# Optimization experiments

Hardware: AMD Instinct MI355X
Metric: run time of the kernel (lower is better)

The kernel has to match this reference:

```python
import jax, jax.numpy as jnp
import numpy as np

N, E = 8192, 131072
NS, NV = 128, 64            # scalar (0e) / vector (1o) multiplicities
D = NS + 3 * NV             # 320 node feature dim
EA = 20                     # edge_attr_dim
HID = 128
WNUM = NS + NS + NV + NV    # 384 per-edge tensor-product weights
EPS = 1e-5


def _split(x):
    return x[:, :NS], x[:, NS:].reshape(x.shape[0], NV, 3)


def _merge(s, v):
    return jnp.concatenate([s, v.reshape(v.shape[0], -1)], axis=-1)


def _o3_linear(x, ws, bs, wv):
    # per-irrep linear: scalars get bias, vectors are channel-mixed only
    s, v = _split(x)
    return _merge(s @ ws + bs, jnp.einsum('ncm,cd->ndm', v, wv))


def _normgate(x):
    # silu on scalars; vectors gated by silu(norm)/norm (equivariant)
    s, v = _split(x)
    n = jnp.sqrt(jnp.sum(v * v, axis=-1) + EPS * EPS)
    return _merge(jax.nn.silu(s), v * (jax.nn.silu(n) / n)[:, :, None])


def setup_inputs() -> dict:
    key = jax.random.key(0)
    ks = jax.random.split(key, 24)
    rn = lambda k, sh, sc=1.0: jax.random.normal(k, sh, dtype=jnp.float32) * sc
    inp = {
        'node_feat': rn(ks[0], (N, D)),
        'edge_attr': rn(ks[1], (E, EA)),
        'edge_rshs': rn(ks[2], (E, 4)),
        'edge_index': jax.random.randint(ks[3], (2, E), 0, N, dtype=jnp.int32),
        # lin_node0 / lin_node1 (o3.Linear on 128x0e+64x1o)
        'lin0_ws': rn(ks[4], (NS, NS), 1 / np.sqrt(NS)),
        'lin0_bs': jnp.zeros((NS,), jnp.float32),
        'lin0_wv': rn(ks[5], (NV, NV), 1 / np.sqrt(NV)),
        'lin1_ws': rn(ks[6], (NS, NS), 1 / np.sqrt(NS)),
        'lin1_bs': jnp.zeros((NS,), jnp.float32),
        'lin1_wv': rn(ks[7], (NV, NV), 1 / np.sqrt(NV)),
        # lin_node2: tp_out (192x0e + 192x1o) -> node_out (128x0e + 64x1o)
        'lin2_ws': rn(ks[8], (NS + NV, NS), 1 / np.sqrt(NS + NV)),
        'lin2_bs': jnp.zeros((NS,), jnp.float32),
        'lin2_wv': rn(ks[9], (NS + NV, NV), 1 / np.sqrt(NS + NV)),
        # lin_edge_scalar MLP: (2*NS + NV = 320) -> 128 -> WNUM
        'es_w1': rn(ks[10], (2 * NS + NV, HID), 1 / np.sqrt(2 * NS + NV)),
        'es_b1': jnp.zeros((HID,), jnp.float32),
        'es_w2': rn(ks[11], (HID, WNUM), 1 / np.sqrt(HID)),
        'es_b2': jnp.zeros((WNUM,), jnp.float32),
        # lin_edge_rbf MLP: EA -> 128 -> WNUM
        'er_w1': rn(ks[12], (EA, HID), 1 / np.sqrt(EA)),
        'er_b1': jnp.zeros((HID,), jnp.float32),
        'er_w2': rn(ks[13], (HID, WNUM), 1 / np.sqrt(HID)),
        'er_b2': jnp.zeros((WNUM,), jnp.float32),
        # EquivariantLayerNorm affine params
        'ln_gs': jnp.ones((NS,), jnp.float32),
        'ln_bs': jnp.zeros((NS,), jnp.float32),
        'ln_gv': jnp.ones((NS + NV,), jnp.float32),
    }
    return inp


def reference(node_feat, edge_attr, edge_rshs, edge_index,
              lin0_ws, lin0_bs, lin0_wv, lin1_ws, lin1_bs, lin1_wv,
              lin2_ws, lin2_bs, lin2_wv,
              es_w1, es_b1, es_w2, es_b2, er_w1, er_b1, er_w2, er_b2,
              ln_gs, ln_bs, ln_gv):
    n_nodes = node_feat.shape[0]
    recv, send = edge_index[0], edge_index[1]

    # lin_node0 + EquivariantDot (keep only the 1o channel dots) -> edge scalars s0
    pre = _o3_linear(node_feat, lin0_ws, lin0_bs, lin0_wv)
    ps, pv = _split(pre)
    vdot = jnp.einsum('ecm,ecm->ec', pv[recv], pv[send])          # [E, NV]
    s0 = jnp.concatenate([ps[recv], ps[send], vdot], axis=-1)     # [E, 320]

    # normgate -> lin_node1 -> gather sender features
    x = _o3_linear(_normgate(node_feat), lin1_ws, lin1_bs, lin1_wv)
    xs, xv = _split(x)
    xs_j, xv_j = xs[send], xv[send]

    # per-edge tensor-product weights: MLP(s0) * MLP(edge_attr)
    w = (jax.nn.silu(s0 @ es_w1 + es_b1) @ es_w2 + es_b2) * \
        (jax.nn.silu(edge_attr @ er_w1 + er_b1) @ er_w2 + er_b2)  # [E, 384]
    w1, w2 = w[:, :NS], w[:, NS:2 * NS]
    w3, w4 = w[:, 2 * NS:2 * NS + NV], w[:, 2 * NS + NV:]

    y0 = edge_rshs[:, :1]    # l=0 SH  [E,1]
    y1 = edge_rshs[:, 1:4]   # l=1 SH  [E,3]

    # uvu weighted tensor product paths (path_normalization='none')
    m_s1 = xs_j * y0 * w1                                                   # 0e x 0e -> 0e [E,NS]
    m_s2 = jnp.einsum('ecm,em->ec', xv_j, y1) * w4 * (1.0 / np.sqrt(3.0))   # 1o x 1o -> 0e [E,NV]
    m_v1 = xs_j[:, :, None] * y1[:, None, :] * w2[:, :, None]               # 0e x 1o -> 1o [E,NS,3]
    m_v2 = xv_j * (y0 * w3)[:, :, None]                                     # 1o x 0e -> 1o [E,NV,3]

    msg_s = jnp.concatenate([m_s1, m_s2], axis=-1)       # [E, NS+NV]
    msg_v = jnp.concatenate([m_v1, m_v2], axis=1)        # [E, NS+NV, 3]

    # scatter-add messages to receiving nodes
    acc_s = jax.ops.segment_sum(msg_s, recv, num_segments=n_nodes)
    acc_v = jax.ops.segment_sum(msg_v, recv, num_segments=n_nodes)

    # lin_node2: mix tp_out channels down to node_out
    os = acc_s @ lin2_ws + lin2_bs                        # [N, NS]
    ov = jnp.einsum('ncm,cd->ndm', acc_v, lin2_wv)        # [N, NV, 3]

    # EquivariantLayerNorm: standard LN on scalars, RMS-of-norms on vectors
    mu = jnp.mean(os, axis=-1, keepdims=True)
    var = jnp.var(os, axis=-1, keepdims=True)
    os = (os - mu) / jnp.sqrt(var + EPS) * ln_gs + ln_bs
    n2 = jnp.mean(jnp.sum(ov * ov, axis=-1), axis=-1, keepdims=True)  # [N,1]
    ov = ov / jnp.sqrt(n2 + EPS)[:, :, None] * ln_gv[NS:][None, :, None]

    # residual update (irreps_in == irreps_out)
    return node_feat + _merge(os, ov)
```

## Files before the change

### kernel.cpp

```cpp
#include <hip/hip_runtime.h>
#include <hip/hip_bf16.h>

typedef __bf16 bf16_t;
typedef __bf16 v8bf __attribute__((ext_vector_type(8)));
typedef __bf16 v2bf __attribute__((ext_vector_type(2)));
typedef __bf16 v4bf __attribute__((ext_vector_type(4)));
typedef float  v16f __attribute__((ext_vector_type(16)));

#define NSC   128
#define NVC   64
#define DDIM  320
#define HIDN  128
#define WNUM  384
#define S0STR 328
#define HSTR  136

__device__ __forceinline__ float siluf(float x) { return x / (1.f + __expf(-x)); }

__global__ void k_wconv(const float* __restrict__ esw1, const float* __restrict__ esw2,
                        const float* __restrict__ erw1, const float* __restrict__ erw2,
                        bf16_t* __restrict__ p1, bf16_t* __restrict__ p2,
                        bf16_t* __restrict__ p3, bf16_t* __restrict__ p4)
{
    const int gid = blockIdx.x * blockDim.x + threadIdx.x;
    const int stride = gridDim.x * blockDim.x;
    for (int i = gid; i < 80*512; i += stride) {
        int frag = i >> 9, q = i & 511, lane = q >> 3, j = q & 7;
        int kc = frag >> 2, nt = frag & 3;
        int n = nt*32 + (lane & 31), k = kc*16 + (lane >> 5)*8 + j;
        p1[i] = (bf16_t)esw1[k*128 + n];
    }
    for (int i = gid; i < 8*512; i += stride) {
        int frag = i >> 9, q = i & 511, lane = q >> 3, j = q & 7;
        int kc = frag >> 2, nt = frag & 3;
        int n = nt*32 + (lane & 31), k = kc*16 + (lane >> 5)*8 + j;
        p3[i] = (k < 20) ? (bf16_t)erw1[k*128 + n] : (bf16_t)(0.f);
    }
    for (int i = gid; i < 96*512; i += stride) {
        int frag = i >> 9, q = i & 511, lane = q >> 3, j = q & 7;
        int ch = frag >> 5, kc = (frag >> 2) & 7, nt = frag & 3;
        int n = ch*128 + nt*32 + (lane & 31), k = kc*16 + (lane >> 5)*8 + j;
        p2[i] = (bf16_t)esw2[k*384 + n];
        p4[i] = (bf16_t)erw2[k*384 + n];
    }
}

__global__ void k_hist(const int* __restrict__ eidx, int* __restrict__ hist, int E)
{
    for (int e = blockIdx.x * blockDim.x + threadIdx.x; e < E; e += gridDim.x * blockDim.x)
        atomicAdd(&hist[eidx[e]], 1);
}

__global__ __launch_bounds__(1024) void k_scan(const int* __restrict__ hist,
                                               int* __restrict__ off, int* __restrict__ cnt, int N)
{
    __shared__ int part[1024];
    const int tid = threadIdx.x;
    const int C = (N + 1023) >> 10;
    const int base = tid * C;
    int s = 0;
    for (int j = 0; j < C; ++j) { int idx = base + j; if (idx < N) s += hist[idx]; }
    part[tid] = s;
    __syncthreads();
    for (int d = 1; d < 1024; d <<= 1) {
        int u = (tid >= d) ? part[tid - d] : 0;
        __syncthreads();
        part[tid] += u;
        __syncthreads();
    }
    int run = part[tid] - s;
    for (int j = 0; j < C; ++j) {
        int idx = base + j;
        if (idx < N) { off[idx] = run; cnt[idx] = run; run += hist[idx]; }
    }
    if (tid == 1023) off[N] = part[1023];
}

__global__ void k_scatter(const int* __restrict__ eidx, const float* __restrict__ rshs,
                          const float* __restrict__ ea_g, int* __restrict__ cnt,
                          int* __restrict__ nsort, int* __restrict__ send_p,
                          float4* __restrict__ rshs_p, bf16_t* __restrict__ ea32, int E)
{
    for (int e = blockIdx.x * blockDim.x + threadIdx.x; e < E; e += gridDim.x * blockDim.x) {
        int n = eidx[e];
        int pos = atomicAdd(&cnt[n], 1);
        nsort[pos] = n;
        send_p[pos] = eidx[E + e];
        rshs_p[pos] = *(const float4*)(rshs + (size_t)e*4);
        const float* src = ea_g + (size_t)e*20;
        bf16_t tmp[32];
        #pragma unroll
        for (int j = 0; j < 20; ++j) tmp[j] = (bf16_t)src[j];
        #pragma unroll
        for (int j = 20; j < 32; ++j) tmp[j] = (bf16_t)(0.f);
        bf16_t* dst = ea32 + (size_t)pos*32;
        #pragma unroll
        for (int q = 0; q < 4; ++q)
            *((v8bf*)dst + q) = *((const v8bf*)tmp + q);
    }
}

__global__ __launch_bounds__(256) void k_nodeprep(
    const float* __restrict__ nf,
    const float* __restrict__ w0s, const float* __restrict__ b0s, const float* __restrict__ w0v,
    const float* __restrict__ w1s, const float* __restrict__ b1s, const float* __restrict__ w1v,
    bf16_t* __restrict__ ps_bf, bf16_t* __restrict__ pv_bf,
    bf16_t* __restrict__ xs_bf, bf16_t* __restrict__ xv4, int N)
{
    __shared__ float s_in[16][128];
    __shared__ float vt[3][64][16];
    const int tid = threadIdx.x;
    const int nb = blockIdx.x * 16;
    const size_t N64 = (size_t)N * 64;

    for (int idx = tid; idx < 16*320; idx += 256) {
        int n = idx / 320, c = idx % 320;
        int gn = nb + n; if (gn >= N) gn = N - 1;
        float v = nf[(size_t)gn*320 + c];
        if (c < 128) s_in[n][c] = v;
        else { int q = c - 128; vt[q % 3][q / 3][n] = v; }
    }
    __syncthreads();

    {
        const int col = tid & 127, g = tid >> 7;
        float acc[8];
        #pragma unroll
        for (int j = 0; j < 8; ++j) acc[j] = 0.f;
        for (int c4 = 0; c4 < 128; c4 += 4) {
            float wa = w0s[(c4+0)*128 + col];
            float wb = w0s[(c4+1)*128 + col];
            float wc = w0s[(c4+2)*128 + col];
            float wd = w0s[(c4+3)*128 + col];
            #pragma unroll
            for (int j = 0; j < 8; ++j) {
                float4 sv = *(const float4*)&s_in[g*8+j][c4];
                acc[j] += sv.x*wa + sv.y*wb + sv.z*wc + sv.w*wd;
            }
        }
        float b = b0s[col];
        #pragma unroll
        for (int j = 0; j < 8; ++j) {
            int gn = nb + g*8 + j;
            if (gn < N) ps_bf[(size_t)gn*128 + col] = (bf16_t)(acc[j] + b);
        }
    }
    if (tid < 192) {
        const int d = tid & 63, m = tid >> 6;
        float acc[16];
        #pragma unroll
        for (int j = 0; j < 16; ++j) acc[j] = 0.f;
        for (int c = 0; c < 64; ++c) {
            float w = w0v[c*64 + d];
            float4 a0 = *(const float4*)&vt[m][c][0];
            float4 a1 = *(const float4*)&vt[m][c][4];
            float4 a2 = *(const float4*)&vt[m][c][8];
            float4 a3 = *(const float4*)&vt[m][c][12];
            acc[0]+=a0.x*w; acc[1]+=a0.y*w; acc[2]+=a0.z*w; acc[3]+=a0.w*w;
            acc[4]+=a1.x*w; acc[5]+=a1.y*w; acc[6]+=a1.z*w; acc[7]+=a1.w*w;
            acc[8]+=a2.x*w; acc[9]+=a2.y*w; acc[10]+=a2.z*w; acc[11]+=a2.w*w;
            acc[12]+=a3.x*w; acc[13]+=a3.y*w; acc[14]+=a3.z*w; acc[15]+=a3.w*w;
        }
        #pragma unroll
        for (int j = 0; j < 16; ++j) {
            int gn = nb + j;
            if (gn < N) pv_bf[(size_t)m*N64 + (size_t)gn*64 + d] = (bf16_t)acc[j];
        }
    }
    __syncthreads();

    for (int idx = tid; idx < 2048; idx += 256) {
        int n = idx >> 7, c = idx & 127;
        s_in[n][c] = siluf(s_in[n][c]);
    }
    for (int idx = tid; idx < 1024; idx += 256) {
        int n = idx & 15, cc = idx >> 4;
        float v0 = vt[0][cc][n], v1 = vt[1][cc][n], v2 = vt[2][cc][n];
        float nn = sqrtf(v0*v0 + v1*v1 + v2*v2 + 1e-10f);
        float sc = 1.f / (1.f + __expf(-nn));
        vt[0][cc][n] = v0*sc; vt[1][cc][n] = v1*sc; vt[2][cc][n] = v2*sc;
    }
    __syncthreads();

    {
        const int col = tid & 127, g = tid >> 7;
        float acc[8];
        #pragma unroll
        for (int j = 0; j < 8; ++j) acc[j] = 0.f;
        for (int c4 = 0; c4 < 128; c4 += 4) {
            float wa = w1s[(c4+0)*128 + col];
            float wb = w1s[(c4+1)*128 + col];
            float wc = w1s[(c4+2)*128 + col];
            float wd = w1s[(c4+3)*128 + col];
            #pragma unroll
            for (int j = 0; j < 8; ++j) {
                float4 sv = *(const float4*)&s_in[g*8+j][c4];
                acc[j] += sv.x*wa + sv.y*wb + sv.z*wc + sv.w*wd;
            }
        }
        float b = b1s[col];
        #pragma unroll
        for (int j = 0; j < 8; ++j) {
            int gn = nb + g*8 + j;
            if (gn < N) xs_bf[(size_t)gn*128 + col] = (bf16_t)(acc[j] + b);
        }
    }
    if (tid < 192) {
        const int d = tid & 63, m = tid >> 6;
        float acc[16];
        #pragma unroll
        for (int j = 0; j < 16; ++j) acc[j] = 0.f;
        for (int c = 0; c < 64; ++c) {
            float w = w1v[c*64 + d];
            float4 a0 = *(const float4*)&vt[m][c][0];
            float4 a1 = *(const float4*)&vt[m][c][4];
            float4 a2 = *(const float4*)&vt[m][c][8];
            float4 a3 = *(const float4*)&vt[m][c][12];
            acc[0]+=a0.x*w; acc[1]+=a0.y*w; acc[2]+=a0.z*w; acc[3]+=a0.w*w;
            acc[4]+=a1.x*w; acc[5]+=a1.y*w; acc[6]+=a1.z*w; acc[7]+=a1.w*w;
            acc[8]+=a2.x*w; acc[9]+=a2.y*w; acc[10]+=a2.z*w; acc[11]+=a2.w*w;
            acc[12]+=a3.x*w; acc[13]+=a3.y*w; acc[14]+=a3.z*w; acc[15]+=a3.w*w;
        }
        #pragma unroll
        for (int j = 0; j < 16; ++j) {
            int gn = nb + j;
            if (gn < N) xv4[(size_t)gn*256 + d*4 + m] = (bf16_t)acc[j];
        }
    }
}

__global__ __launch_bounds__(256) void k_edge2(
    const int* __restrict__ nsort, const int* __restrict__ send_p,
    const bf16_t* __restrict__ ea32,
    const bf16_t* __restrict__ ps_bf, const bf16_t* __restrict__ pv_bf,
    const bf16_t* __restrict__ p1, const bf16_t* __restrict__ p2,
    const bf16_t* __restrict__ p3, const bf16_t* __restrict__ p4,
    const float* __restrict__ es_b1, const float* __restrict__ es_b2,
    const float* __restrict__ er_b1, const float* __restrict__ er_b2,
    bf16_t* __restrict__ w_bf, int N, int E)
{
    __shared__ __align__(16) bf16_t s0h[32*S0STR];
    __shared__ int   recv_l[32], send_l[32];

    const int tid  = threadIdx.x;
    const int lane = tid & 63;
    const int wid  = tid >> 6;
    const int e0   = blockIdx.x * 32;
    const size_t N64 = (size_t)N * 64;

    if (tid < 32) {
        int i = e0 + tid; if (i >= E) i = E - 1;
        recv_l[tid] = nsort[i];
        send_l[tid] = send_p[i];
    }
    __syncthreads();

    #pragma unroll
    for (int rr = 0; rr < 8; ++rr) {
        int r = wid*8 + rr;
        int nr = recv_l[r], nsd = send_l[r];
        if (lane < 32) {
            *(uint2*)&s0h[r*S0STR + lane*4] = *(const uint2*)(ps_bf + (size_t)nr*NSC + lane*4);
        } else {
            int l2 = lane - 32;
            *(uint2*)&s0h[r*S0STR + 128 + l2*4] = *(const uint2*)(ps_bf + (size_t)nsd*NSC + l2*4);
        }
        float d = 0.f;
        #pragma unroll
        for (int m = 0; m < 3; ++m)
            d += (float)pv_bf[m*N64 + (size_t)nr*64 + lane] * (float)pv_bf[m*N64 + (size_t)nsd*64 + lane];
        s0h[r*S0STR + 256 + lane] = (bf16_t)d;
    }
    __syncthreads();

    const int lc = lane & 31;
    const int kh = lane >> 5;
    bf16_t* h1 = s0h;
    bf16_t* h2 = s0h + 32*HSTR;
    const int col1 = wid*32 + lc;

    v16f acc;

    #pragma unroll
    for (int j = 0; j < 16; ++j) acc[j] = 0.f;
    {
        const bf16_t* aB = &s0h[lc*S0STR + kh*8];
        #pragma unroll
        for (int kc = 0; kc < 20; ++kc) {
            v8bf a = *(const v8bf*)(aB + kc*16);
            v8bf b = *(const v8bf*)(p1 + (size_t)((kc<<2) + wid)*512 + lane*8);
            acc = __builtin_amdgcn_mfma_f32_32x32x16_bf16(a, b, acc, 0, 0, 0);
        }
    }
    __syncthreads();

    {
        const float be = es_b1[col1];
        #pragma unroll
        for (int reg = 0; reg < 16; ++reg) {
            int row = (reg & 3) + 8*(reg >> 2) + 4*kh;
            h1[row*HSTR + col1] = (bf16_t)siluf(acc[reg] + be);
        }
    }

    #pragma unroll
    for (int j = 0; j < 16; ++j) acc[j] = 0.f;
    #pragma unroll
    for (int kc = 0; kc < 2; ++kc) {
        v8bf a = *(const v8bf*)(ea32 + (size_t)(e0 + lc)*32 + kc*16 + kh*8);
        v8bf b = *(const v8bf*)(p3 + (size_t)((kc<<2) + wid)*512 + lane*8);
        acc = __builtin_amdgcn_mfma_f32_32x32x16_bf16(a, b, acc, 0, 0, 0);
    }
    {
        const float br = er_b1[col1];
        #pragma unroll
        for (int reg = 0; reg < 16; ++reg) {
            int row = (reg & 3) + 8*(reg >> 2) + 4*kh;
            h2[row*HSTR + col1] = (bf16_t)siluf(acc[reg] + br);
        }
    }
    __syncthreads();

    #pragma unroll
    for (int ch = 0; ch < 3; ++ch) {
        #pragma unroll
        for (int j = 0; j < 16; ++j) acc[j] = 0.f;
        #pragma unroll
        for (int kc = 0; kc < 8; ++kc) {
            v8bf a1 = *(const v8bf*)&h1[lc*HSTR + kc*16 + kh*8];
            v8bf b1 = *(const v8bf*)(p2 + (size_t)(((ch*8 + kc)<<2) + wid)*512 + lane*8);
            acc = __builtin_amdgcn_mfma_f32_32x32x16_bf16(a1, b1, acc, 0, 0, 0);
        }
        const int col = ch*128 + wid*32 + lc;
        const float be = es_b2[col];
        bf16_t hes[16];
        #pragma unroll
        for (int reg = 0; reg < 16; ++reg) hes[reg] = (bf16_t)(acc[reg] + be);

        #pragma unroll
        for (int j = 0; j < 16; ++j) acc[j] = 0.f;
        #pragma unroll
        for (int kc = 0; kc < 8; ++kc) {
            v8bf a2 = *(const v8bf*)&h2[lc*HSTR + kc*16 + kh*8];
            v8bf b2 = *(const v8bf*)(p4 + (size_t)(((ch*8 + kc)<<2) + wid)*512 + lane*8);
            acc = __builtin_amdgcn_mfma_f32_32x32x16_bf16(a2, b2, acc, 0, 0, 0);
        }
        const float br = er_b2[col];
        int idx;
        if (ch == 0)      idx = col*2;
        else if (ch == 1) idx = (col - 128)*2 + 1;
        else { int q = col - 256; idx = (q < 64) ? 256 + q*2 : 256 + (q - 64)*2 + 1; }
        #pragma unroll
        for (int reg = 0; reg < 16; ++reg) {
            int row = (reg & 3) + 8*(reg >> 2) + 4*kh;
            int i = e0 + row;
            if (i < E) w_bf[(size_t)i*WNUM + idx] = (bf16_t)((float)hes[reg] * (acc[reg] + br));
        }
    }
}

__global__ __launch_bounds__(192) void k_gather(
    const int* __restrict__ off, const int* __restrict__ send_p,
    const float4* __restrict__ rshs_p,
    const bf16_t* __restrict__ xs_bf, const bf16_t* __restrict__ xv4,
    const bf16_t* __restrict__ w_bf,
    const float* __restrict__ nf,
    const float* __restrict__ w2s, const float* __restrict__ b2s, const float* __restrict__ w2v,
    const float* __restrict__ ln_gs, const float* __restrict__ ln_bs, const float* __restrict__ ln_gv,
    float* __restrict__ out, int N, int E)
{
    __shared__ float accS_l[192];
    __shared__ float accV_l[576];
    __shared__ float os_l[128];
    __shared__ float ov_l[192];
    __shared__ float stats[3];
    const int tid = threadIdx.x;
    const int n = blockIdx.x;
    const int i0 = off[n], i1 = off[n+1];

    float a0 = 0.f, a1 = 0.f, a2 = 0.f, a3 = 0.f;
    float b0 = 0.f, b1 = 0.f, b2 = 0.f, b3 = 0.f;
    if (tid < 128) {
        const int c = tid;
        int i = i0;
        for (; i + 2 <= i1; i += 2) {
            int nsdA = send_p[i],   nsdB = send_p[i+1];
            float4 yA = rshs_p[i],  yB = rshs_p[i+1];
            v2bf wA = *(const v2bf*)(w_bf + (size_t)i*WNUM + c*2);
            v2bf wB = *(const v2bf*)(w_bf + (size_t)(i+1)*WNUM + c*2);
            float xsA = (float)xs_bf[(size_t)nsdA*NSC + c];
            float xsB = (float)xs_bf[(size_t)nsdB*NSC + c];
            a0 += xsA * yA.x * (float)wA[0];
            b0 += xsB * yB.x * (float)wB[0];
            float xwA = xsA * (float)wA[1], xwB = xsB * (float)wB[1];
            a1 += xwA * yA.y; a2 += xwA * yA.z; a3 += xwA * yA.w;
            b1 += xwB * yB.y; b2 += xwB * yB.z; b3 += xwB * yB.w;
        }
        if (i < i1) {
            int nsd = send_p[i];
            float4 y = rshs_p[i];
            v2bf w = *(const v2bf*)(w_bf + (size_t)i*WNUM + c*2);
            float xs = (float)xs_bf[(size_t)nsd*NSC + c];
            a0 += xs * y.x * (float)w[0];
            float xw = xs * (float)w[1];
            a1 += xw * y.y; a2 += xw * y.z; a3 += xw * y.w;
        }
        a0 += b0; a1 += b1; a2 += b2; a3 += b3;
        accS_l[c] = a0;
        accV_l[c*3+0] = a1; accV_l[c*3+1] = a2; accV_l[c*3+2] = a3;
    } else {
        const int u = tid - 128;
        int i = i0;
        for (; i + 2 <= i1; i += 2) {
            int nsdA = send_p[i],   nsdB = send_p[i+1];
            float4 yA = rshs_p[i],  yB = rshs_p[i+1];
            v2bf wA = *(const v2bf*)(w_bf + (size_t)i*WNUM + 256 + u*2);
            v2bf wB = *(const v2bf*)(w_bf + (size_t)(i+1)*WNUM + 256 + u*2);
            v4bf xvA = *(const v4bf*)(xv4 + (size_t)nsdA*256 + u*4);
            v4bf xvB = *(const v4bf*)(xv4 + (size_t)nsdB*256 + u*4);
            float vA0 = (float)xvA[0], vA1 = (float)xvA[1], vA2 = (float)xvA[2];
            float vB0 = (float)xvB[0], vB1 = (float)xvB[1], vB2 = (float)xvB[2];
            a0 += (vA0*yA.y + vA1*yA.z + vA2*yA.w) * (float)wA[1] * 0.57735026918962576f;
            b0 += (vB0*yB.y + vB1*yB.z + vB2*yB.w) * (float)wB[1] * 0.57735026918962576f;
            float sA = yA.x * (float)wA[0], sB = yB.x * (float)wB[0];
            a1 += vA0*sA; a2 += vA1*sA; a3 += vA2*sA;
            b1 += vB0*sB; b2 += vB1*sB; b3 += vB2*sB;
        }
        if (i < i1) {
            int nsd = send_p[i];
            float4 y = rshs_p[i];
            v2bf w = *(const v2bf*)(w_bf + (size_t)i*WNUM + 256 + u*2);
            v4bf xv = *(const v4bf*)(xv4 + (size_t)nsd*256 + u*4);
            float v0 = (float)xv[0], v1 = (float)xv[1], v2 = (float)xv[2];
            a0 += (v0*y.y + v1*y.z + v2*y.w) * (float)w[1] * 0.57735026918962576f;
            float s = y.x * (float)w[0];
            a1 += v0*s; a2 += v1*s; a3 += v2*s;
        }
        a0 += b0; a1 += b1; a2 += b2; a3 += b3;
        accS_l[128+u] = a0;
        accV_l[(128+u)*3+0] = a1; accV_l[(128+u)*3+1] = a2; accV_l[(128+u)*3+2] = a3;
    }
    __syncthreads();

    for (int o = tid; o < 320; o += 192) {
        if (o < 128) {
            float acc = 0.f;
            #pragma unroll 4
            for (int c = 0; c < 192; ++c) acc += accS_l[c] * w2s[c*128 + o];
            os_l[o] = acc + b2s[o];
        } else {
            int q = o - 128;
            int m = q % 3, d = q / 3;
            float acc = 0.f;
            #pragma unroll 4
            for (int c = 0; c < 192; ++c) acc += accV_l[c*3 + m] * w2v[c*64 + d];
            ov_l[q] = acc;
        }
    }
    __syncthreads();

    if (tid < 64) {
        float x0 = os_l[tid], x1 = os_l[tid + 64];
        float s = x0 + x1;
        #pragma unroll
        for (int o = 32; o > 0; o >>= 1) s += __shfl_xor(s, o);
        float mu = s * (1.f/128.f);
        float d0 = x0 - mu, d1 = x1 - mu;
        float q = d0*d0 + d1*d1;
        #pragma unroll
        for (int o = 32; o > 0; o >>= 1) q += __shfl_xor(q, o);
        float var = q * (1.f/128.f);
        float v0 = ov_l[tid], v1 = ov_l[tid + 64], v2 = ov_l[tid + 128];
        float q2 = v0*v0 + v1*v1 + v2*v2;
        #pragma unroll
        for (int o = 32; o > 0; o >>= 1) q2 += __shfl_xor(q2, o);
        float n2 = q2 * (1.f/64.f);
        if (tid == 0) {
            stats[0] = mu;
            stats[1] = rsqrtf(var + 1e-5f);
            stats[2] = rsqrtf(n2 + 1e-5f);
        }
    }
    __syncthreads();

    const float mu = stats[0], rstd = stats[1], rn2 = stats[2];
    const size_t base = (size_t)n * DDIM;
    for (int i = tid; i < DDIM; i += 192) {
        if (i < 128) {
            out[base + i] = nf[base + i] + (os_l[i] - mu) * rstd * ln_gs[i] + ln_bs[i];
        } else {
            int o = i - 128;
            int d = o / 3;
            out[base + i] = nf[base + i] + ov_l[o] * rn2 * ln_gv[128 + d];
        }
    }
}

static inline size_t align64(size_t x) { return (x + 63) & ~(size_t)63; }

extern "C" void kernel_launch(void* const* d_in, const int* in_sizes, int n_in,
                              void* d_out, int out_size, void* d_ws, size_t ws_size,
                              hipStream_t stream)
{
    const float* nf    = (const float*)d_in[0];
    const float* ea_g  = (const float*)d_in[1];
    const float* rshs  = (const float*)d_in[2];
    const int*   eidx  = (const int*)  d_in[3];
    const float* w0s   = (const float*)d_in[4];
    const float* b0s   = (const float*)d_in[5];
    const float* w0v   = (const float*)d_in[6];
    const float* w1s   = (const float*)d_in[7];
    const float* b1s   = (const float*)d_in[8];
    const float* w1v   = (const float*)d_in[9];
    const float* w2s   = (const float*)d_in[10];
    const float* b2s   = (const float*)d_in[11];
    const float* w2v   = (const float*)d_in[12];
    const float* esw1  = (const float*)d_in[13];
    const float* esb1  = (const float*)d_in[14];
    const float* esw2  = (const float*)d_in[15];
    const float* esb2  = (const float*)d_in[16];
    const float* erw1  = (const float*)d_in[17];
    const float* erb1  = (const float*)d_in[18];
    const float* erw2  = (const float*)d_in[19];
    const float* erb2  = (const float*)d_in[20];
    const float* ln_gs = (const float*)d_in[21];
    const float* ln_bs = (const float*)d_in[22];
    const float* ln_gv = (const float*)d_in[23];

    const int N = in_sizes[0] / DDIM;
    const int E = in_sizes[3] / 2;

    char* p = (char*)d_ws;
    size_t o = 0;
    int* hist = (int*)(p + o);  o = align64(o + (size_t)N * 4);
    int* off  = (int*)(p + o);  o = align64(o + (size_t)(N + 1) * 4);
    int* cnt  = (int*)(p + o);  o = align64(o + (size_t)N * 4);
    int* nsort= (int*)(p + o);  o = align64(o + (size_t)E * 4);
    int* send_p = (int*)(p + o); o = align64(o + (size_t)E * 4);
    float4* rshs_p = (float4*)(p + o); o = align64(o + (size_t)E * 16);
    bf16_t* ea32 = (bf16_t*)(p + o); o = align64(o + (size_t)(E + 64) * 32 * 2);
    bf16_t* ps_bf = (bf16_t*)(p + o); o = align64(o + (size_t)N * 128 * 2);
    bf16_t* pv_bf = (bf16_t*)(p + o); o = align64(o + (size_t)N * 192 * 2);
    bf16_t* xs_bf = (bf16_t*)(p + o); o = align64(o + (size_t)N * 128 * 2);
    bf16_t* xv4  = (bf16_t*)(p + o); o = align64(o + (size_t)N * 256 * 2);
    bf16_t* p1 = (bf16_t*)(p + o); o = align64(o + (size_t)80 * 512 * 2);
    bf16_t* p2 = (bf16_t*)(p + o); o = align64(o + (size_t)96 * 512 * 2);
    bf16_t* p3 = (bf16_t*)(p + o); o = align64(o + (size_t)8  * 512 * 2);
    bf16_t* p4 = (bf16_t*)(p + o); o = align64(o + (size_t)96 * 512 * 2);
    bf16_t* w_bf  = (bf16_t*)(p + o); o = align64(o + (size_t)E * WNUM * 2);

    hipMemsetAsync(hist, 0, (size_t)N * 4, stream);
    k_wconv<<<64, 256, 0, stream>>>(esw1, esw2, erw1, erw2, p1, p2, p3, p4);
    k_nodeprep<<<(N + 15)/16, 256, 0, stream>>>(nf, w0s, b0s, w0v, w1s, b1s, w1v,
                                                ps_bf, pv_bf, xs_bf, xv4, N);
    k_hist<<<256, 256, 0, stream>>>(eidx, hist, E);
    k_scan<<<1, 1024, 0, stream>>>(hist, off, cnt, N);
    k_scatter<<<512, 256, 0, stream>>>(eidx, rshs, ea_g, cnt,
                                       nsort, send_p, rshs_p, ea32, E);
    k_edge2<<<(E + 31)/32, 256, 0, stream>>>(nsort, send_p, ea32, ps_bf, pv_bf,
                                             p1, p2, p3, p4,
                                             esb1, esb2, erb1, erb2, w_bf, N, E);
    k_gather<<<N, 192, 0, stream>>>(off, send_p, rshs_p, xs_bf, xv4, w_bf,
                                    nf, w2s, b2s, w2v, ln_gs, ln_bs, ln_gv,
                                    (float*)d_out, N, E);
}
```

Before: 320.1 us.

## Fuse message computation and scatter into edge MLP kernel via atomics

The per-edge tensor-product weights are no longer written to a global E×384 bf16 buffer and re-read by a per-node gather kernel. The edge MLP kernel now multiplies each weight by the gathered sender features and spherical harmonics directly in registers. It reduces consecutive rows that share a receiver (edges are sorted by receiver) and issues float atomicAdds into zeroed per-node accumulators. A lighter node-output kernel then only loads those accumulators. This removes the large weight-buffer round trip, but adds global atomics, a memset of the accumulators, and scattered feature gathers inside the MFMA kernel.

```diff
diff --git a/kernel.cpp b/kernel.cpp
--- a/kernel.cpp
+++ b/kernel.cpp
@@ -231,16 +231,19 @@
 
 __global__ __launch_bounds__(256) void k_edge2(
     const int* __restrict__ nsort, const int* __restrict__ send_p,
+    const float4* __restrict__ rshs_p,
     const bf16_t* __restrict__ ea32,
     const bf16_t* __restrict__ ps_bf, const bf16_t* __restrict__ pv_bf,
+    const bf16_t* __restrict__ xs_bf, const bf16_t* __restrict__ xv4,
     const bf16_t* __restrict__ p1, const bf16_t* __restrict__ p2,
     const bf16_t* __restrict__ p3, const bf16_t* __restrict__ p4,
     const float* __restrict__ es_b1, const float* __restrict__ es_b2,
     const float* __restrict__ er_b1, const float* __restrict__ er_b2,
-    bf16_t* __restrict__ w_bf, int N, int E)
+    float* __restrict__ accS, float* __restrict__ accV, int N, int E)
 {
     __shared__ __align__(16) bf16_t s0h[32*S0STR];
     __shared__ int   recv_l[32], send_l[32];
+    __shared__ float4 y_l[32];
 
     const int tid  = threadIdx.x;
     const int lane = tid & 63;
@@ -252,6 +255,7 @@
         int i = e0 + tid; if (i >= E) i = E - 1;
         recv_l[tid] = nsort[i];
         send_l[tid] = send_p[i];
+        y_l[tid]    = rshs_p[i];
     }
     __syncthreads();
 
@@ -346,28 +350,98 @@
             acc = __builtin_amdgcn_mfma_f32_32x32x16_bf16(a2, b2, acc, 0, 0, 0);
         }
         const float br = er_b2[col];
-        int idx;
-        if (ch == 0)      idx = col*2;
-        else if (ch == 1) idx = (col - 128)*2 + 1;
-        else { int q = col - 256; idx = (q < 64) ? 256 + q*2 : 256 + (q - 64)*2 + 1; }
-        #pragma unroll
-        for (int reg = 0; reg < 16; ++reg) {
-            int row = (reg & 3) + 8*(reg >> 2) + 4*kh;
-            int i = e0 + row;
-            if (i < E) w_bf[(size_t)i*WNUM + idx] = (bf16_t)((float)hes[reg] * (acc[reg] + br));
-        }
-    }
-}
-
-__global__ __launch_bounds__(192) void k_gather(
-    const int* __restrict__ off, const int* __restrict__ send_p,
-    const float4* __restrict__ rshs_p,
-    const bf16_t* __restrict__ xs_bf, const bf16_t* __restrict__ xv4,
-    const bf16_t* __restrict__ w_bf,
+
+        if (ch == 0) {
+            const int c = col;
+            float sum = 0.f;
+            int cur = recv_l[4*kh];
+            #pragma unroll
+            for (int reg = 0; reg < 16; ++reg) {
+                int row = (reg & 3) + 8*(reg >> 2) + 4*kh;
+                int nr = recv_l[row];
+                if (nr != cur) { atomicAdd(accS + (size_t)cur*192 + c, sum); sum = 0.f; cur = nr; }
+                if (e0 + row < E) {
+                    float wv = (float)hes[reg] * (acc[reg] + br);
+                    float xs = (float)xs_bf[(size_t)send_l[row]*NSC + c];
+                    sum += xs * y_l[row].x * wv;
+                }
+            }
+            atomicAdd(accS + (size_t)cur*192 + c, sum);
+        } else if (ch == 1) {
+            const int c = col - 128;
+            float s0 = 0.f, s1 = 0.f, s2 = 0.f;
+            int cur = recv_l[4*kh];
+            #pragma unroll
+            for (int reg = 0; reg < 16; ++reg) {
+                int row = (reg & 3) + 8*(reg >> 2) + 4*kh;
+                int nr = recv_l[row];
+                if (nr != cur) {
+                    float* bp = accV + (size_t)cur*576 + c*3;
+                    atomicAdd(bp+0, s0); atomicAdd(bp+1, s1); atomicAdd(bp+2, s2);
+                    s0 = s1 = s2 = 0.f; cur = nr;
+                }
+                if (e0 + row < E) {
+                    float wv = (float)hes[reg] * (acc[reg] + br);
+                    float xs = (float)xs_bf[(size_t)send_l[row]*NSC + c];
+                    float xw = xs * wv;
+                    float4 y = y_l[row];
+                    s0 += xw * y.y; s1 += xw * y.z; s2 += xw * y.w;
+                }
+            }
+            float* bp = accV + (size_t)cur*576 + c*3;
+            atomicAdd(bp+0, s0); atomicAdd(bp+1, s1); atomicAdd(bp+2, s2);
+        } else {
+            const int q = col - 256;
+            if (q < 64) {
+                const int u = q;
+                float s0 = 0.f, s1 = 0.f, s2 = 0.f;
+                int cur = recv_l[4*kh];
+                #pragma unroll
+                for (int reg = 0; reg < 16; ++reg) {
+                    int row = (reg & 3) + 8*(reg >> 2) + 4*kh;
+                    int nr = recv_l[row];
+                    if (nr != cur) {
+                        float* bp = accV + (size_t)cur*576 + (128+u)*3;
+                        atomicAdd(bp+0, s0); atomicAdd(bp+1, s1); atomicAdd(bp+2, s2);
+                        s0 = s1 = s2 = 0.f; cur = nr;
+                    }
+                    if (e0 + row < E) {
+                        float wv = (float)hes[reg] * (acc[reg] + br);
+                        v4bf xv = *(const v4bf*)(xv4 + (size_t)send_l[row]*256 + u*4);
+                        float s = y_l[row].x * wv;
+                        s0 += (float)xv[0]*s; s1 += (float)xv[1]*s; s2 += (float)xv[2]*s;
+                    }
+                }
+                float* bp = accV + (size_t)cur*576 + (128+u)*3;
+                atomicAdd(bp+0, s0); atomicAdd(bp+1, s1); atomicAdd(bp+2, s2);
+            } else {
+                const int u = q - 64;
+                float sum = 0.f;
+                int cur = recv_l[4*kh];
+                #pragma unroll
+                for (int reg = 0; reg < 16; ++reg) {
+                    int row = (reg & 3) + 8*(reg >> 2) + 4*kh;
+                    int nr = recv_l[row];
+                    if (nr != cur) { atomicAdd(accS + (size_t)cur*192 + 128 + u, sum); sum = 0.f; cur = nr; }
+                    if (e0 + row < E) {
+                        float wv = (float)hes[reg] * (acc[reg] + br);
+                        v4bf xv = *(const v4bf*)(xv4 + (size_t)send_l[row]*256 + u*4);
+                        float4 y = y_l[row];
+                        sum += ((float)xv[0]*y.y + (float)xv[1]*y.z + (float)xv[2]*y.w) * wv * 0.57735026918962576f;
+                    }
+                }
+                atomicAdd(accS + (size_t)cur*192 + 128 + u, sum);
+            }
+        }
+    }
+}
+
+__global__ __launch_bounds__(192) void k_nodeout(
+    const float* __restrict__ accS, const float* __restrict__ accV,
     const float* __restrict__ nf,
     const float* __restrict__ w2s, const float* __restrict__ b2s, const float* __restrict__ w2v,
     const float* __restrict__ ln_gs, const float* __restrict__ ln_bs, const float* __restrict__ ln_gv,
-    float* __restrict__ out, int N, int E)
+    float* __restrict__ out, int N)
 {
     __shared__ float accS_l[192];
     __shared__ float accV_l[576];
@@ -376,70 +450,9 @@
     __shared__ float stats[3];
     const int tid = threadIdx.x;
     const int n = blockIdx.x;
-    const int i0 = off[n], i1 = off[n+1];
-
-    float a0 = 0.f, a1 = 0.f, a2 = 0.f, a3 = 0.f;
-    float b0 = 0.f, b1 = 0.f, b2 = 0.f, b3 = 0.f;
-    if (tid < 128) {
-        const int c = tid;
-        int i = i0;
-        for (; i + 2 <= i1; i += 2) {
-            int nsdA = send_p[i],   nsdB = send_p[i+1];
-            float4 yA = rshs_p[i],  yB = rshs_p[i+1];
-            v2bf wA = *(const v2bf*)(w_bf + (size_t)i*WNUM + c*2);
-            v2bf wB = *(const v2bf*)(w_bf + (size_t)(i+1)*WNUM + c*2);
-            float xsA = (float)xs_bf[(size_t)nsdA*NSC + c];
-            float xsB = (float)xs_bf[(size_t)nsdB*NSC + c];
-            a0 += xsA * yA.x * (float)wA[0];
-            b0 += xsB * yB.x * (float)wB[0];
-            float xwA = xsA * (float)wA[1], xwB = xsB * (float)wB[1];
-            a1 += xwA * yA.y; a2 += xwA * yA.z; a3 += xwA * yA.w;
-            b1 += xwB * yB.y; b2 += xwB * yB.z; b3 += xwB * yB.w;
-        }
-        if (i < i1) {
-            int nsd = send_p[i];
-            float4 y = rshs_p[i];
-            v2bf w = *(const v2bf*)(w_bf + (size_t)i*WNUM + c*2);
-            float xs = (float)xs_bf[(size_t)nsd*NSC + c];
-            a0 += xs * y.x * (float)w[0];
-            float xw = xs * (float)w[1];
-            a1 += xw * y.y; a2 += xw * y.z; a3 += xw * y.w;
-        }
-        a0 += b0; a1 += b1; a2 += b2; a3 += b3;
-        accS_l[c] = a0;
-        accV_l[c*3+0] = a1; accV_l[c*3+1] = a2; accV_l[c*3+2] = a3;
-    } else {
-        const int u = tid - 128;
-        int i = i0;
-        for (; i + 2 <= i1; i += 2) {
-            int nsdA = send_p[i],   nsdB = send_p[i+1];
-            float4 yA = rshs_p[i],  yB = rshs_p[i+1];
-            v2bf wA = *(const v2bf*)(w_bf + (size_t)i*WNUM + 256 + u*2);
-            v2bf wB = *(const v2bf*)(w_bf + (size_t)(i+1)*WNUM + 256 + u*2);
-            v4bf xvA = *(const v4bf*)(xv4 + (size_t)nsdA*256 + u*4);
-            v4bf xvB = *(const v4bf*)(xv4 + (size_t)nsdB*256 + u*4);
-            float vA0 = (float)xvA[0], vA1 = (float)xvA[1], vA2 = (float)xvA[2];
-            float vB0 = (float)xvB[0], vB1 = (float)xvB[1], vB2 = (float)xvB[2];
-            a0 += (vA0*yA.y + vA1*yA.z + vA2*yA.w) * (float)wA[1] * 0.57735026918962576f;
-            b0 += (vB0*yB.y + vB1*yB.z + vB2*yB.w) * (float)wB[1] * 0.57735026918962576f;
-            float sA = yA.x * (float)wA[0], sB = yB.x * (float)wB[0];
-            a1 += vA0*sA; a2 += vA1*sA; a3 += vA2*sA;
-            b1 += vB0*sB; b2 += vB1*sB; b3 += vB2*sB;
-        }
-        if (i < i1) {
-            int nsd = send_p[i];
-            float4 y = rshs_p[i];
-            v2bf w = *(const v2bf*)(w_bf + (size_t)i*WNUM + 256 + u*2);
-            v4bf xv = *(const v4bf*)(xv4 + (size_t)nsd*256 + u*4);
-            float v0 = (float)xv[0], v1 = (float)xv[1], v2 = (float)xv[2];
-            a0 += (v0*y.y + v1*y.z + v2*y.w) * (float)w[1] * 0.57735026918962576f;
-            float s = y.x * (float)w[0];
-            a1 += v0*s; a2 += v1*s; a3 += v2*s;
-        }
-        a0 += b0; a1 += b1; a2 += b2; a3 += b3;
-        accS_l[128+u] = a0;
-        accV_l[(128+u)*3+0] = a1; accV_l[(128+u)*3+1] = a2; accV_l[(128+u)*3+2] = a3;
-    }
+
+    for (int i = tid; i < 192; i += 192) accS_l[i] = accS[(size_t)n*192 + i];
+    for (int i = tid; i < 576; i += 192) accV_l[i] = accV[(size_t)n*576 + i];
     __syncthreads();
 
     for (int o = tid; o < 320; o += 192) {
@@ -532,6 +545,8 @@
 
     char* p = (char*)d_ws;
     size_t o = 0;
+    float* accS = (float*)(p + o); o = align64(o + (size_t)N * 192 * 4);
+    float* accV = (float*)(p + o); o = align64(o + (size_t)N * 576 * 4);
     int* hist = (int*)(p + o);  o = align64(o + (size_t)N * 4);
     int* off  = (int*)(p + o);  o = align64(o + (size_t)(N + 1) * 4);
     int* cnt  = (int*)(p + o);  o = align64(o + (size_t)N * 4);
@@ -547,8 +562,8 @@
     bf16_t* p2 = (bf16_t*)(p + o); o = align64(o + (size_t)96 * 512 * 2);
     bf16_t* p3 = (bf16_t*)(p + o); o = align64(o + (size_t)8  * 512 * 2);
     bf16_t* p4 = (bf16_t*)(p + o); o = align64(o + (size_t)96 * 512 * 2);
-    bf16_t* w_bf  = (bf16_t*)(p + o); o = align64(o + (size_t)E * WNUM * 2);
-
+
+    hipMemsetAsync(accS, 0, (size_t)N * 768 * 4, stream);
     hipMemsetAsync(hist, 0, (size_t)N * 4, stream);
     k_wconv<<<64, 256, 0, stream>>>(esw1, esw2, erw1, erw2, p1, p2, p3, p4);
     k_nodeprep<<<(N + 15)/16, 256, 0, stream>>>(nf, w0s, b0s, w0v, w1s, b1s, w1v,
@@ -557,10 +572,9 @@
     k_scan<<<1, 1024, 0, stream>>>(hist, off, cnt, N);
     k_scatter<<<512, 256, 0, stream>>>(eidx, rshs, ea_g, cnt,
                                        nsort, send_p, rshs_p, ea32, E);
-    k_edge2<<<(E + 31)/32, 256, 0, stream>>>(nsort, send_p, ea32, ps_bf, pv_bf,
-                                             p1, p2, p3, p4,
-                                             esb1, esb2, erb1, erb2, w_bf, N, E);
-    k_gather<<<N, 192, 0, stream>>>(off, send_p, rshs_p, xs_bf, xv4, w_bf,
-                                    nf, w2s, b2s, w2v, ln_gs, ln_bs, ln_gv,
-                                    (float*)d_out, N, E);
-}
+    k_edge2<<<(E + 31)/32, 256, 0, stream>>>(nsort, send_p, rshs_p, ea32, ps_bf, pv_bf,
+                                             xs_bf, xv4, p1, p2, p3, p4,
+                                             esb1, esb2, erb1, erb2, accS, accV, N, E);
+    k_nodeout<<<N, 192, 0, stream>>>(accS, accV, nf, w2s, b2s, w2v,
+                                     ln_gs, ln_bs, ln_gv, (float*)d_out, N);
+}
```

Result: slower. 438.9 us (+37.1%).

## Process four nodes per gather block to reuse lin2 weights; fuse histogram into wconv

Applied to the files above, without the earlier changes.

The gather kernel now handles GNB=4 nodes per block. Each lin_node2 weight loaded from global memory is applied to all four nodes' accumulators, cutting weight traffic per node by four, and the layer-norm reductions are spread across the three wavefronts. The edge histogram is folded into the weight-conversion kernel, which now launches with more blocks, removing one kernel launch. The cost is fewer blocks, more shared memory per block, and serialized edge gathering over the four nodes, which may reduce latency hiding in the gather phase.

```diff
diff --git a/kernel.cpp b/kernel.cpp
--- a/kernel.cpp
+++ b/kernel.cpp
@@ -14,13 +14,15 @@
 #define WNUM  384
 #define S0STR 328
 #define HSTR  136
+#define GNB   4
 
 __device__ __forceinline__ float siluf(float x) { return x / (1.f + __expf(-x)); }
 
 __global__ void k_wconv(const float* __restrict__ esw1, const float* __restrict__ esw2,
                         const float* __restrict__ erw1, const float* __restrict__ erw2,
                         bf16_t* __restrict__ p1, bf16_t* __restrict__ p2,
-                        bf16_t* __restrict__ p3, bf16_t* __restrict__ p4)
+                        bf16_t* __restrict__ p3, bf16_t* __restrict__ p4,
+                        const int* __restrict__ eidx, int* __restrict__ hist, int E)
 {
     const int gid = blockIdx.x * blockDim.x + threadIdx.x;
     const int stride = gridDim.x * blockDim.x;
@@ -43,11 +45,7 @@
         p2[i] = (bf16_t)esw2[k*384 + n];
         p4[i] = (bf16_t)erw2[k*384 + n];
     }
-}
-
-__global__ void k_hist(const int* __restrict__ eidx, int* __restrict__ hist, int E)
-{
-    for (int e = blockIdx.x * blockDim.x + threadIdx.x; e < E; e += gridDim.x * blockDim.x)
+    for (int e = gid; e < E; e += stride)
         atomicAdd(&hist[eidx[e]], 1);
 }
 
@@ -369,129 +367,152 @@
     const float* __restrict__ ln_gs, const float* __restrict__ ln_bs, const float* __restrict__ ln_gv,
     float* __restrict__ out, int N, int E)
 {
-    __shared__ float accS_l[192];
-    __shared__ float accV_l[576];
-    __shared__ float os_l[128];
-    __shared__ float ov_l[192];
-    __shared__ float stats[3];
+    __shared__ float accS_l[GNB][192];
+    __shared__ float accV_l[GNB][576];
+    __shared__ float os_l[GNB][128];
+    __shared__ float ov_l[GNB][192];
+    __shared__ float stats[GNB][3];
     const int tid = threadIdx.x;
-    const int n = blockIdx.x;
-    const int i0 = off[n], i1 = off[n+1];
-
-    float a0 = 0.f, a1 = 0.f, a2 = 0.f, a3 = 0.f;
-    float b0 = 0.f, b1 = 0.f, b2 = 0.f, b3 = 0.f;
-    if (tid < 128) {
-        const int c = tid;
-        int i = i0;
-        for (; i + 2 <= i1; i += 2) {
-            int nsdA = send_p[i],   nsdB = send_p[i+1];
-            float4 yA = rshs_p[i],  yB = rshs_p[i+1];
-            v2bf wA = *(const v2bf*)(w_bf + (size_t)i*WNUM + c*2);
-            v2bf wB = *(const v2bf*)(w_bf + (size_t)(i+1)*WNUM + c*2);
-            float xsA = (float)xs_bf[(size_t)nsdA*NSC + c];
-            float xsB = (float)xs_bf[(size_t)nsdB*NSC + c];
-            a0 += xsA * yA.x * (float)wA[0];
-            b0 += xsB * yB.x * (float)wB[0];
-            float xwA = xsA * (float)wA[1], xwB = xsB * (float)wB[1];
-            a1 += xwA * yA.y; a2 += xwA * yA.z; a3 += xwA * yA.w;
-            b1 += xwB * yB.y; b2 += xwB * yB.z; b3 += xwB * yB.w;
-        }
-        if (i < i1) {
-            int nsd = send_p[i];
-            float4 y = rshs_p[i];
-            v2bf w = *(const v2bf*)(w_bf + (size_t)i*WNUM + c*2);
-            float xs = (float)xs_bf[(size_t)nsd*NSC + c];
-            a0 += xs * y.x * (float)w[0];
-            float xw = xs * (float)w[1];
-            a1 += xw * y.y; a2 += xw * y.z; a3 += xw * y.w;
-        }
-        a0 += b0; a1 += b1; a2 += b2; a3 += b3;
-        accS_l[c] = a0;
-        accV_l[c*3+0] = a1; accV_l[c*3+1] = a2; accV_l[c*3+2] = a3;
-    } else {
-        const int u = tid - 128;
-        int i = i0;
-        for (; i + 2 <= i1; i += 2) {
-            int nsdA = send_p[i],   nsdB = send_p[i+1];
-            float4 yA = rshs_p[i],  yB = rshs_p[i+1];
-            v2bf wA = *(const v2bf*)(w_bf + (size_t)i*WNUM + 256 + u*2);
-            v2bf wB = *(const v2bf*)(w_bf + (size_t)(i+1)*WNUM + 256 + u*2);
-            v4bf xvA = *(const v4bf*)(xv4 + (size_t)nsdA*256 + u*4);
-            v4bf xvB = *(const v4bf*)(xv4 + (size_t)nsdB*256 + u*4);
-            float vA0 = (float)xvA[0], vA1 = (float)xvA[1], vA2 = (float)xvA[2];
-            float vB0 = (float)xvB[0], vB1 = (float)xvB[1], vB2 = (float)xvB[2];
-            a0 += (vA0*yA.y + vA1*yA.z + vA2*yA.w) * (float)wA[1] * 0.57735026918962576f;
-            b0 += (vB0*yB.y + vB1*yB.z + vB2*yB.w) * (float)wB[1] * 0.57735026918962576f;
-            float sA = yA.x * (float)wA[0], sB = yB.x * (float)wB[0];
-            a1 += vA0*sA; a2 += vA1*sA; a3 += vA2*sA;
-            b1 += vB0*sB; b2 += vB1*sB; b3 += vB2*sB;
-        }
-        if (i < i1) {
-            int nsd = send_p[i];
-            float4 y = rshs_p[i];
-            v2bf w = *(const v2bf*)(w_bf + (size_t)i*WNUM + 256 + u*2);
-            v4bf xv = *(const v4bf*)(xv4 + (size_t)nsd*256 + u*4);
-            float v0 = (float)xv[0], v1 = (float)xv[1], v2 = (float)xv[2];
-            a0 += (v0*y.y + v1*y.z + v2*y.w) * (float)w[1] * 0.57735026918962576f;
-            float s = y.x * (float)w[0];
-            a1 += v0*s; a2 += v1*s; a3 += v2*s;
-        }
-        a0 += b0; a1 += b1; a2 += b2; a3 += b3;
-        accS_l[128+u] = a0;
-        accV_l[(128+u)*3+0] = a1; accV_l[(128+u)*3+1] = a2; accV_l[(128+u)*3+2] = a3;
+    const int nb = blockIdx.x * GNB;
+
+    for (int nn = 0; nn < GNB; ++nn) {
+        int node = nb + nn;
+        int i0 = 0, i1 = 0;
+        if (node < N) { i0 = off[node]; i1 = off[node+1]; }
+        float a0 = 0.f, a1 = 0.f, a2 = 0.f, a3 = 0.f;
+        float b0 = 0.f, b1 = 0.f, b2 = 0.f, b3 = 0.f;
+        if (tid < 128) {
+            const int c = tid;
+            int i = i0;
+            for (; i + 2 <= i1; i += 2) {
+                int nsdA = send_p[i],   nsdB = send_p[i+1];
+                float4 yA = rshs_p[i],  yB = rshs_p[i+1];
+                v2bf wA = *(const v2bf*)(w_bf + (size_t)i*WNUM + c*2);
+                v2bf wB = *(const v2bf*)(w_bf + (size_t)(i+1)*WNUM + c*2);
+                float xsA = (float)xs_bf[(size_t)nsdA*NSC + c];
+                float xsB = (float)xs_bf[(size_t)nsdB*NSC + c];
+                a0 += xsA * yA.x * (float)wA[0];
+                b0 += xsB * yB.x * (float)wB[0];
+                float xwA = xsA * (float)wA[1], xwB = xsB * (float)wB[1];
+                a1 += xwA * yA.y; a2 += xwA * yA.z; a3 += xwA * yA.w;
+                b1 += xwB * yB.y; b2 += xwB * yB.z; b3 += xwB * yB.w;
+            }
+            if (i < i1) {
+                int nsd = send_p[i];
+                float4 y = rshs_p[i];
+                v2bf w = *(const v2bf*)(w_bf + (size_t)i*WNUM + c*2);
+                float xs = (float)xs_bf[(size_t)nsd*NSC + c];
+                a0 += xs * y.x * (float)w[0];
+                float xw = xs * (float)w[1];
+                a1 += xw * y.y; a2 += xw * y.z; a3 += xw * y.w;
+            }
+            a0 += b0; a1 += b1; a2 += b2; a3 += b3;
+            accS_l[nn][c] = a0;
+            accV_l[nn][c*3+0] = a1; accV_l[nn][c*3+1] = a2; accV_l[nn][c*3+2] = a3;
+        } else {
+            const int u = tid - 128;
+            int i = i0;
+            for (; i + 2 <= i1; i += 2) {
+                int nsdA = send_p[i],   nsdB = send_p[i+1];
+                float4 yA = rshs_p[i],  yB = rshs_p[i+1];
+                v2bf wA = *(const v2bf*)(w_bf + (size_t)i*WNUM + 256 + u*2);
+                v2bf wB = *(const v2bf*)(w_bf + (size_t)(i+1)*WNUM + 256 + u*2);
+                v4bf xvA = *(const v4bf*)(xv4 + (size_t)nsdA*256 + u*4);
+                v4bf xvB = *(const v4bf*)(xv4 + (size_t)nsdB*256 + u*4);
+                float vA0 = (float)xvA[0], vA1 = (float)xvA[1], vA2 = (float)xvA[2];
+                float vB0 = (float)xvB[0], vB1 = (float)xvB[1], vB2 = (float)xvB[2];
+                a0 += (vA0*yA.y + vA1*yA.z + vA2*yA.w) * (float)wA[1] * 0.57735026918962576f;
+                b0 += (vB0*yB.y + vB1*yB.z + vB2*yB.w) * (float)wB[1] * 0.57735026918962576f;
+                float sA = yA.x * (float)wA[0], sB = yB.x * (float)wB[0];
+                a1 += vA0*sA; a2 += vA1*sA; a3 += vA2*sA;
+                b1 += vB0*sB; b2 += vB1*sB; b3 += vB2*sB;
+            }
+            if (i < i1) {
+                int nsd = send_p[i];
+                float4 y = rshs_p[i];
+                v2bf w = *(const v2bf*)(w_bf + (size_t)i*WNUM + 256 + u*2);
+                v4bf xv = *(const v4bf*)(xv4 + (size_t)nsd*256 + u*4);
+                float v0 = (float)xv[0], v1 = (float)xv[1], v2 = (float)xv[2];
+                a0 += (v0*y.y + v1*y.z + v2*y.w) * (float)w[1] * 0.57735026918962576f;
+                float s = y.x * (float)w[0];
+                a1 += v0*s; a2 += v1*s; a3 += v2*s;
+            }
+            a0 += b0; a1 += b1; a2 += b2; a3 += b3;
+            accS_l[nn][128+u] = a0;
+            accV_l[nn][(128+u)*3+0] = a1; accV_l[nn][(128+u)*3+1] = a2; accV_l[nn][(128+u)*3+2] = a3;
+        }
     }
     __syncthreads();
 
     for (int o = tid; o < 320; o += 192) {
         if (o < 128) {
-            float acc = 0.f;
-            #pragma unroll 4
-            for (int c = 0; c < 192; ++c) acc += accS_l[c] * w2s[c*128 + o];
-            os_l[o] = acc + b2s[o];
+            float acc[GNB];
+            #pragma unroll
+            for (int nn = 0; nn < GNB; ++nn) acc[nn] = 0.f;
+            for (int c = 0; c < 192; ++c) {
+                float w = w2s[c*128 + o];
+                #pragma unroll
+                for (int nn = 0; nn < GNB; ++nn) acc[nn] += accS_l[nn][c] * w;
+            }
+            float b = b2s[o];
+            #pragma unroll
+            for (int nn = 0; nn < GNB; ++nn) os_l[nn][o] = acc[nn] + b;
         } else {
             int q = o - 128;
             int m = q % 3, d = q / 3;
-            float acc = 0.f;
-            #pragma unroll 4
-            for (int c = 0; c < 192; ++c) acc += accV_l[c*3 + m] * w2v[c*64 + d];
-            ov_l[q] = acc;
-        }
-    }
-    __syncthreads();
-
-    if (tid < 64) {
-        float x0 = os_l[tid], x1 = os_l[tid + 64];
-        float s = x0 + x1;
-        #pragma unroll
-        for (int o = 32; o > 0; o >>= 1) s += __shfl_xor(s, o);
-        float mu = s * (1.f/128.f);
-        float d0 = x0 - mu, d1 = x1 - mu;
-        float q = d0*d0 + d1*d1;
-        #pragma unroll
-        for (int o = 32; o > 0; o >>= 1) q += __shfl_xor(q, o);
-        float var = q * (1.f/128.f);
-        float v0 = ov_l[tid], v1 = ov_l[tid + 64], v2 = ov_l[tid + 128];
-        float q2 = v0*v0 + v1*v1 + v2*v2;
-        #pragma unroll
-        for (int o = 32; o > 0; o >>= 1) q2 += __shfl_xor(q2, o);
-        float n2 = q2 * (1.f/64.f);
-        if (tid == 0) {
-            stats[0] = mu;
-            stats[1] = rsqrtf(var + 1e-5f);
-            stats[2] = rsqrtf(n2 + 1e-5f);
-        }
-    }
-    __syncthreads();
-
-    const float mu = stats[0], rstd = stats[1], rn2 = stats[2];
-    const size_t base = (size_t)n * DDIM;
-    for (int i = tid; i < DDIM; i += 192) {
-        if (i < 128) {
-            out[base + i] = nf[base + i] + (os_l[i] - mu) * rstd * ln_gs[i] + ln_bs[i];
+            float acc[GNB];
+            #pragma unroll
+            for (int nn = 0; nn < GNB; ++nn) acc[nn] = 0.f;
+            for (int c = 0; c < 192; ++c) {
+                float w = w2v[c*64 + d];
+                #pragma unroll
+                for (int nn = 0; nn < GNB; ++nn) acc[nn] += accV_l[nn][c*3 + m] * w;
+            }
+            #pragma unroll
+            for (int nn = 0; nn < GNB; ++nn) ov_l[nn][q] = acc[nn];
+        }
+    }
+    __syncthreads();
+
+    {
+        const int lane = tid & 63, wv = tid >> 6;
+        for (int nn = wv; nn < GNB; nn += 3) {
+            float x0 = os_l[nn][lane], x1 = os_l[nn][lane + 64];
+            float s = x0 + x1;
+            #pragma unroll
+            for (int o = 32; o > 0; o >>= 1) s += __shfl_xor(s, o);
+            float mu = s * (1.f/128.f);
+            float d0 = x0 - mu, d1 = x1 - mu;
+            float q = d0*d0 + d1*d1;
+            #pragma unroll
+            for (int o = 32; o > 0; o >>= 1) q += __shfl_xor(q, o);
+            float var = q * (1.f/128.f);
+            float v0 = ov_l[nn][lane], v1 = ov_l[nn][lane + 64], v2 = ov_l[nn][lane + 128];
+            float q2 = v0*v0 + v1*v1 + v2*v2;
+            #pragma unroll
+            for (int o = 32; o > 0; o >>= 1) q2 += __shfl_xor(q2, o);
+            float n2 = q2 * (1.f/64.f);
+            if (lane == 0) {
+                stats[nn][0] = mu;
+                stats[nn][1] = rsqrtf(var + 1e-5f);
+                stats[nn][2] = rsqrtf(n2 + 1e-5f);
+            }
+        }
+    }
+    __syncthreads();
+
+    for (int i = tid; i < GNB*DDIM; i += 192) {
+        int nn = i / DDIM, j = i % DDIM;
+        int node = nb + nn;
+        if (node >= N) continue;
+        const float mu = stats[nn][0], rstd = stats[nn][1], rn2 = stats[nn][2];
+        const size_t base = (size_t)node * DDIM;
+        if (j < 128) {
+            out[base + j] = nf[base + j] + (os_l[nn][j] - mu) * rstd * ln_gs[j] + ln_bs[j];
         } else {
-            int o = i - 128;
+            int o = j - 128;
             int d = o / 3;
-            out[base + i] = nf[base + i] + ov_l[o] * rn2 * ln_gv[128 + d];
+            out[base + j] = nf[base + j] + ov_l[nn][o] * rn2 * ln_gv[128 + d];
         }
     }
 }
@@ -550,17 +571,16 @@
     bf16_t* w_bf  = (bf16_t*)(p + o); o = align64(o + (size_t)E * WNUM * 2);
 
     hipMemsetAsync(hist, 0, (size_t)N * 4, stream);
-    k_wconv<<<64, 256, 0, stream>>>(esw1, esw2, erw1, erw2, p1, p2, p3, p4);
+    k_wconv<<<512, 256, 0, stream>>>(esw1, esw2, erw1, erw2, p1, p2, p3, p4, eidx, hist, E);
     k_nodeprep<<<(N + 15)/16, 256, 0, stream>>>(nf, w0s, b0s, w0v, w1s, b1s, w1v,
                                                 ps_bf, pv_bf, xs_bf, xv4, N);
-    k_hist<<<256, 256, 0, stream>>>(eidx, hist, E);
     k_scan<<<1, 1024, 0, stream>>>(hist, off, cnt, N);
     k_scatter<<<512, 256, 0, stream>>>(eidx, rshs, ea_g, cnt,
                                        nsort, send_p, rshs_p, ea32, E);
     k_edge2<<<(E + 31)/32, 256, 0, stream>>>(nsort, send_p, ea32, ps_bf, pv_bf,
                                              p1, p2, p3, p4,
                                              esb1, esb2, erb1, erb2, w_bf, N, E);
-    k_gather<<<N, 192, 0, stream>>>(off, send_p, rshs_p, xs_bf, xv4, w_bf,
-                                    nf, w2s, b2s, w2v, ln_gs, ln_bs, ln_gv,
-                                    (float*)d_out, N, E);
-}
+    k_gather<<<(N + GNB - 1)/GNB, 192, 0, stream>>>(off, send_p, rshs_p, xs_bf, xv4, w_bf,
+                                                    nf, w2s, b2s, w2v, ln_gs, ln_bs, ln_gv,
+                                                    (float*)d_out, N, E);
+}
```

After: 268.5 us. 16.1% less time.
